# Performance work log

Measured on AMD Instinct MI355X. Metric: run time of the kernel, lower is better.

The kernel has to match this reference:

```python
import jax, jax.numpy as jnp
import numpy as np

INPUT_SIZE = 512
HIDDEN_SIZE = 1024
BATCH = 64
SEQ = 512


def _xavier(key, shape):
    fan_in, fan_out = shape
    limit = float(np.sqrt(6.0 / (fan_in + fan_out)))
    return jax.random.uniform(key, shape, jnp.float32, -limit, limit)


def setup_inputs() -> dict:
    key = jax.random.key(0)
    ks = jax.random.split(key, 9)
    x = jax.random.normal(ks[0], (BATCH, SEQ, INPUT_SIZE), jnp.float32)
    # gate order: i, f, g, o
    W_x = jnp.stack([_xavier(ks[1 + j], (INPUT_SIZE, HIDDEN_SIZE)) for j in range(4)])   # [4, I, H]
    W_h = jnp.stack([_xavier(ks[5 + j], (HIDDEN_SIZE, HIDDEN_SIZE)) for j in range(4)])  # [4, H, H]
    b = jnp.zeros((4, HIDDEN_SIZE), jnp.float32)  # init_weights zeros all biases
    return {"x": x, "W_x": W_x, "W_h": W_h, "b": b}


def reference(x, W_x, W_h, b):
    """x: [B,S,I]; W_x: [4,I,H]; W_h: [4,H,H]; b: [4,H]. Returns final (h, c)."""
    B = x.shape[0]
    H = W_h.shape[-1]
    # Fuse the 4 input-side GEMMs across all timesteps into one big GEMM.
    # xg[t] : [B, 4, H]
    xg = jnp.einsum('bsi,gih->sbgh', x, W_x) + b  # [S, B, 4, H]

    W_h_cat = jnp.transpose(W_h, (1, 0, 2)).reshape(H, 4 * H)  # [H, 4H], gate-major blocks

    def step(carry, xg_t):
        h_prev, c_prev = carry
        gates = xg_t + (h_prev @ W_h_cat).reshape(B, 4, H)  # [B,4,H]
        i_t = jax.nn.sigmoid(gates[:, 0])
        f_t = jax.nn.sigmoid(gates[:, 1])
        g_t = jnp.tanh(gates[:, 2])
        o_t = jax.nn.sigmoid(gates[:, 3])
        c_t = f_t * c_prev + i_t * g_t
        h_t = o_t * jnp.tanh(c_t)
        return (h_t, c_t), None

    h0 = jnp.zeros((B, H), x.dtype)
    c0 = jnp.zeros((B, H), x.dtype)
    (h_T, c_T), _ = jax.lax.scan(step, (h0, c0), xg)
    return h_T, c_T
```

## Files before the change

kernel.cpp:

```cpp
#include <hip/hip_runtime.h>
#include <hip/hip_bf16.h>
#include <stdint.h>
#include <stddef.h>

#define ISZ   512
#define HSZ   1024
#define NBAT  64
#define SEQL  512

typedef __attribute__((ext_vector_type(8))) short  short8;
typedef __attribute__((ext_vector_type(4))) float  floatx4;

__device__ __forceinline__ unsigned short f2bf(float f){
  unsigned int u = __float_as_uint(f);
  u += 0x7FFFu + ((u >> 16) & 1u);
  return (unsigned short)(u >> 16);
}
__device__ __forceinline__ float sigf(float x){ return 1.0f / (1.0f + __expf(-x)); }
__device__ __forceinline__ float tanh_(float x){ return 2.0f / (1.0f + __expf(-2.0f * x)) - 1.0f; }
__device__ __forceinline__ float sel4(int idx, float a0, float a1, float a2, float a3){
  float r01 = (idx & 1) ? a1 : a0;
  float r23 = (idx & 1) ? a3 : a2;
  return (idx & 2) ? r23 : r01;
}

__global__ __launch_bounds__(256) void k_convert_x(const float* __restrict__ x,
                                                   unsigned short* __restrict__ xb,
                                                   int* __restrict__ flags){
  if (blockIdx.x == 0 && threadIdx.x < 256) flags[threadIdx.x] = 0;
  int i = (blockIdx.x * 256 + threadIdx.x) * 8;
  const float4* p = (const float4*)(x + i);
  float4 a = p[0], b = p[1];
  unsigned int w0 = (unsigned int)f2bf(a.x) | ((unsigned int)f2bf(a.y) << 16);
  unsigned int w1 = (unsigned int)f2bf(a.z) | ((unsigned int)f2bf(a.w) << 16);
  unsigned int w2 = (unsigned int)f2bf(b.x) | ((unsigned int)f2bf(b.y) << 16);
  unsigned int w3 = (unsigned int)f2bf(b.z) | ((unsigned int)f2bf(b.w) << 16);
  *(uint4*)(xb + i) = make_uint4(w0, w1, w2, w3);
}

__global__ __launch_bounds__(256) void k_pack_w(const float* __restrict__ Wx,
                                                const float* __restrict__ Wh,
                                                unsigned short* __restrict__ pw){
  int id = blockIdx.x * 256 + threadIdx.x;
  int lane = id & 63;
  int ch   = (id >> 6) % 48;
  int t2   = (id >> 6) / 48;
  int wv = t2 & 3, cg = t2 >> 2;
  int nn = lane & 15, kgrp = lane >> 4;
  int g = nn >> 2, hcl = nn & 3;
  int colh = cg * 16 + wv * 4 + hcl;
  unsigned short o[8];
  if (ch < 32){
    int k0 = ch * 32 + kgrp * 8;
#pragma unroll
    for (int j = 0; j < 8; ++j) o[j] = f2bf(Wh[(g * 1024 + k0 + j) * 1024 + colh]);
  } else {
    int k0 = (ch - 32) * 32 + kgrp * 8;
#pragma unroll
    for (int j = 0; j < 8; ++j) o[j] = f2bf(Wx[(g * 512 + k0 + j) * 1024 + colh]);
  }
  unsigned int w0 = (unsigned int)o[0] | ((unsigned int)o[1] << 16);
  unsigned int w1 = (unsigned int)o[2] | ((unsigned int)o[3] << 16);
  unsigned int w2 = (unsigned int)o[4] | ((unsigned int)o[5] << 16);
  unsigned int w3 = (unsigned int)o[6] | ((unsigned int)o[7] << 16);
  ((uint4*)pw)[id] = make_uint4(w0, w1, w2, w3);
}

__global__ __launch_bounds__(256, 1) void k_scan(const unsigned short* __restrict__ pw,
                                                 const unsigned short* __restrict__ xb,
                                                 const float* __restrict__ bias,
                                                 unsigned long long* __restrict__ hgq,
                                                 int* __restrict__ flags,
                                                 float* __restrict__ out){
  __shared__ __align__(16) char lds_h[16 * 2048];
  __shared__ __align__(16) char lds_x[16 * 1024];

  const int wg = blockIdx.x;
  const int bg = wg >> 6;
  const int cg = wg & 63;
  const int tid = threadIdx.x;
  const int wv = tid >> 6;
  const int lane = tid & 63;
  const int b0 = bg * 16;

  short8 bh[32], bx[16];
  {
    const uint4* base = (const uint4*)pw + (cg * 4 + wv) * 48 * 64 + lane;
#pragma unroll
    for (int c = 0; c < 32; ++c) bh[c] = *(const short8*)(base + c * 64);
#pragma unroll
    for (int c = 0; c < 16; ++c) bx[c] = *(const short8*)(base + (32 + c) * 64);
  }
#pragma unroll
  for (int c = 0; c < 32; ++c) asm volatile("" : "+v"(bh[c]));
#pragma unroll
  for (int c = 0; c < 16; ++c) asm volatile("" : "+v"(bx[c]));

  const int nn = lane & 15;
  const int G  = nn >> 2;
  const int hc = nn & 3;
  const int kgrp = lane >> 4;
  const int colh = cg * 16 + wv * 4 + hc;
  const float b_i = bias[0 * HSZ + colh];
  const float b_f = bias[1 * HSZ + colh];
  const float b_g = bias[2 * HSZ + colh];
  const float b_o = bias[3 * HSZ + colh];

  const int arow = nn;
  const int swz  = (arow & 7) << 4;
  const int hb0  = arow * 2048 + ((kgrp * 16 +  0) ^ swz);
  const int hb1  = arow * 2048 + ((kgrp * 16 + 64) ^ swz);
  const int xq0  = arow * 1024 + ((kgrp * 16 +  0) ^ swz);
  const int xq1  = arow * 1024 + ((kgrp * 16 + 64) ^ swz);

  float cst[4] = {0.f, 0.f, 0.f, 0.f};

#pragma unroll 1
  for (int t = 0; t < SEQL; ++t){
    uint4 xr[4]; int xdst[4];
#pragma unroll
    for (int i = 0; i < 4; ++i){
      int ch = i * 256 + tid;
      int row = ch >> 6, o16 = ch & 63;
      xr[i] = *(const uint4*)((const char*)xb + (((size_t)(b0 + row) * SEQL + t) * ISZ) * 2 + o16 * 16);
      xdst[i] = row * 1024 + ((o16 * 16) ^ ((row & 7) << 4));
    }

    if (t > 0){
      if (wv == 0){
        const int need = 4 * t;
        const int fidx = bg * 64 + lane;
        for (;;){
          int f = __hip_atomic_load(&flags[fidx], __ATOMIC_RELAXED, __HIP_MEMORY_SCOPE_AGENT);
          if (__all(f >= need)) break;
          __builtin_amdgcn_s_sleep(1);
        }
      }
      __syncthreads();
    }

    if (t > 0){
      unsigned long long hr[16]; int hdst[16];
      const int par_r = (t - 1) & 1;
#pragma unroll
      for (int i = 0; i < 16; ++i){
        int ch = i * 256 + tid;
        int row = ch >> 8, o8 = ch & 255;
        hr[i] = __hip_atomic_load(hgq + ((size_t)(par_r * 64 + b0 + row)) * 256 + o8,
                                  __ATOMIC_RELAXED, __HIP_MEMORY_SCOPE_AGENT);
        hdst[i] = row * 2048 + ((o8 * 8) ^ ((row & 7) << 4));
      }
#pragma unroll
      for (int i = 0; i < 16; ++i) *(unsigned long long*)(lds_h + hdst[i]) = hr[i];
    }
#pragma unroll
    for (int i = 0; i < 4; ++i) *(uint4*)(lds_x + xdst[i]) = xr[i];
    __syncthreads();

    floatx4 acc0 = {0.f, 0.f, 0.f, 0.f};
    floatx4 acc1 = {0.f, 0.f, 0.f, 0.f};
    if (t > 0){
#pragma unroll
      for (int q = 0; q < 16; ++q){
        short8 a0 = *(const short8*)(lds_h + hb0 + q * 128);
        acc0 = __builtin_amdgcn_mfma_f32_16x16x32_bf16(a0, bh[2 * q], acc0, 0, 0, 0);
        short8 a1 = *(const short8*)(lds_h + hb1 + q * 128);
        acc1 = __builtin_amdgcn_mfma_f32_16x16x32_bf16(a1, bh[2 * q + 1], acc1, 0, 0, 0);
      }
    }
#pragma unroll
    for (int q = 0; q < 8; ++q){
      short8 a0 = *(const short8*)(lds_x + xq0 + q * 128);
      acc0 = __builtin_amdgcn_mfma_f32_16x16x32_bf16(a0, bx[2 * q], acc0, 0, 0, 0);
      short8 a1 = *(const short8*)(lds_x + xq1 + q * 128);
      acc1 = __builtin_amdgcn_mfma_f32_16x16x32_bf16(a1, bx[2 * q + 1], acc1, 0, 0, 0);
    }

    float hvv[4];
#pragma unroll
    for (int r = 0; r < 4; ++r){
      float own = acc0[r] + acc1[r];
      float s4  = __shfl_xor(own, 4);
      float s8  = __shfl_xor(own, 8);
      float s12 = __shfl_xor(own, 12);
      float pi = sel4(G,     own, s4, s8, s12) + b_i;
      float pf = sel4(G ^ 1, own, s4, s8, s12) + b_f;
      float pg = sel4(G ^ 2, own, s4, s8, s12) + b_g;
      float po = sel4(G ^ 3, own, s4, s8, s12) + b_o;
      float iv = sigf(pi), fv = sigf(pf), gv = tanh_(pg), ov = sigf(po);
      float cn = fv * cst[r] + iv * gv;
      cst[r] = cn;
      hvv[r] = ov * tanh_(cn);
      if (G == 0 && t == SEQL - 1){
        int gb = b0 + kgrp * 4 + r;
        out[gb * HSZ + colh] = hvv[r];
        out[NBAT * HSZ + gb * HSZ + colh] = cn;
      }
    }

    if (G == 0){
      float a0 = hvv[0], a1 = hvv[1], a2 = hvv[2], a3 = hvv[3];
      float s0 = __shfl_xor(a1, 1), s1 = __shfl_xor(a0, 1);
      float s2 = __shfl_xor(a3, 1), s3 = __shfl_xor(a2, 1);
      bool o1 = (nn & 1);
      float t0 = o1 ? s0 : a0,  t1 = o1 ? a1 : s1;
      float t2 = o1 ? s2 : a2,  t3 = o1 ? a3 : s3;
      float u0 = __shfl_xor(t2, 2), u1 = __shfl_xor(t3, 2);
      float u2 = __shfl_xor(t0, 2), u3 = __shfl_xor(t1, 2);
      bool o2 = (nn & 2);
      float w0 = o2 ? u0 : t0,  w1 = o2 ? u1 : t1;
      float w2 = o2 ? t2 : u2,  w3 = o2 ? t3 : u3;
      unsigned int lo = (unsigned int)f2bf(w0) | ((unsigned int)f2bf(w1) << 16);
      unsigned int hi = (unsigned int)f2bf(w2) | ((unsigned int)f2bf(w3) << 16);
      unsigned long long v = ((unsigned long long)hi << 32) | lo;
      int row = kgrp * 4 + nn;
      __hip_atomic_store(hgq + ((size_t)((t & 1) * 64 + b0 + row)) * 256 + (cg * 4 + wv), v,
                         __ATOMIC_RELAXED, __HIP_MEMORY_SCOPE_AGENT);
    }
    asm volatile("s_waitcnt vmcnt(0)" ::: "memory");
    if (lane == 0)
      __hip_atomic_fetch_add(&flags[wg], 1, __ATOMIC_RELAXED, __HIP_MEMORY_SCOPE_AGENT);
  }
}

extern "C" void kernel_launch(void* const* d_in, const int* in_sizes, int n_in,
                              void* d_out, int out_size, void* d_ws, size_t ws_size,
                              hipStream_t stream){
  (void)in_sizes; (void)n_in; (void)out_size; (void)ws_size;
  const float* x  = (const float*)d_in[0];
  const float* Wx = (const float*)d_in[1];
  const float* Wh = (const float*)d_in[2];
  const float* b  = (const float*)d_in[3];
  char* ws = (char*)d_ws;
  unsigned short* pw    = (unsigned short*)ws;
  unsigned short* xbf   = (unsigned short*)(ws + 12582912);
  unsigned long long* hg= (unsigned long long*)(ws + 46137344);
  int*            flags = (int*)(ws + 46399488);
  float* out = (float*)d_out;

  k_convert_x<<<dim3(8192), dim3(256), 0, stream>>>(x, xbf, flags);
  k_pack_w  <<<dim3(3072), dim3(256), 0, stream>>>(Wx, Wh, pw);
  k_scan    <<<dim3(256),  dim3(256), 0, stream>>>(pw, xbf, b, (unsigned long long*)hg, flags, out);
}
```

Measured before the change: 3.157 ms.

## Replace flag-counter barrier with timestep-tagged h exchange and prefetch x projection

The per-step synchronisation changes. Each block no longer bumps a flag counter that consumers poll before loading h. Each bf16 h value is now stored with a 16-bit timestep tag, and consumers spin on the data words until the tags match. The input-projection MFMAs for the next timestep are computed at the end of the current step, which takes them off the h-dependent critical path. The cost is a doubled h exchange footprint. The flag reset also goes away, so stale tags left in the workspace from a previous launch could match early and be read as valid.

After: 7.005 ms. +121.9%, slower.

```diff
diff --git a/kernel.cpp b/kernel.cpp
--- a/kernel.cpp
+++ b/kernel.cpp
@@ -25,9 +25,7 @@
 }
 
 __global__ __launch_bounds__(256) void k_convert_x(const float* __restrict__ x,
-                                                   unsigned short* __restrict__ xb,
-                                                   int* __restrict__ flags){
-  if (blockIdx.x == 0 && threadIdx.x < 256) flags[threadIdx.x] = 0;
+                                                   unsigned short* __restrict__ xb){
   int i = (blockIdx.x * 256 + threadIdx.x) * 8;
   const float4* p = (const float4*)(x + i);
   float4 a = p[0], b = p[1];
@@ -69,8 +67,7 @@
 __global__ __launch_bounds__(256, 1) void k_scan(const unsigned short* __restrict__ pw,
                                                  const unsigned short* __restrict__ xb,
                                                  const float* __restrict__ bias,
-                                                 unsigned long long* __restrict__ hgq,
-                                                 int* __restrict__ flags,
+                                                 unsigned long long* __restrict__ hq,
                                                  float* __restrict__ out){
   __shared__ __align__(16) char lds_h[16 * 2048];
   __shared__ __align__(16) char lds_x[16 * 1024];
@@ -113,52 +110,74 @@
   const int xq0  = arow * 1024 + ((kgrp * 16 +  0) ^ swz);
   const int xq1  = arow * 1024 + ((kgrp * 16 + 64) ^ swz);
 
+  const int prow = tid >> 4;
+  const int pcb  = (tid & 15) * 64;
+  const int pswz = (prow & 7) << 4;
+
   float cst[4] = {0.f, 0.f, 0.f, 0.f};
-
-#pragma unroll 1
-  for (int t = 0; t < SEQL; ++t){
-    uint4 xr[4]; int xdst[4];
+  floatx4 xp0, xp1;
+
+  {
 #pragma unroll
     for (int i = 0; i < 4; ++i){
       int ch = i * 256 + tid;
       int row = ch >> 6, o16 = ch & 63;
-      xr[i] = *(const uint4*)((const char*)xb + (((size_t)(b0 + row) * SEQL + t) * ISZ) * 2 + o16 * 16);
+      uint4 v = *(const uint4*)((const char*)xb + (((size_t)(b0 + row) * SEQL + 0) * ISZ) * 2 + o16 * 16);
+      *(uint4*)(lds_x + row * 1024 + ((o16 * 16) ^ ((row & 7) << 4))) = v;
+    }
+    __syncthreads();
+    floatx4 a0v = {0.f,0.f,0.f,0.f}, a1v = {0.f,0.f,0.f,0.f};
+#pragma unroll
+    for (int q = 0; q < 8; ++q){
+      short8 a0 = *(const short8*)(lds_x + xq0 + q * 128);
+      a0v = __builtin_amdgcn_mfma_f32_16x16x32_bf16(a0, bx[2 * q], a0v, 0, 0, 0);
+      short8 a1 = *(const short8*)(lds_x + xq1 + q * 128);
+      a1v = __builtin_amdgcn_mfma_f32_16x16x32_bf16(a1, bx[2 * q + 1], a1v, 0, 0, 0);
+    }
+    xp0 = a0v; xp1 = a1v;
+    __syncthreads();
+  }
+
+#pragma unroll 1
+  for (int t = 0; t < SEQL; ++t){
+    const int tn = (t + 1 < SEQL) ? (t + 1) : (SEQL - 1);
+    uint4 xr[4]; int xdst[4];
+#pragma unroll
+    for (int i = 0; i < 4; ++i){
+      int ch = i * 256 + tid;
+      int row = ch >> 6, o16 = ch & 63;
+      xr[i] = *(const uint4*)((const char*)xb + (((size_t)(b0 + row) * SEQL + tn) * ISZ) * 2 + o16 * 16);
       xdst[i] = row * 1024 + ((o16 * 16) ^ ((row & 7) << 4));
     }
 
     if (t > 0){
-      if (wv == 0){
-        const int need = 4 * t;
-        const int fidx = bg * 64 + lane;
-        for (;;){
-          int f = __hip_atomic_load(&flags[fidx], __ATOMIC_RELAXED, __HIP_MEMORY_SCOPE_AGENT);
-          if (__all(f >= need)) break;
-          __builtin_amdgcn_s_sleep(1);
+      const unsigned int tg = (unsigned int)(t - 1);
+      unsigned long long* base = hq + ((size_t)(((t - 1) & 1) * 64 + b0 + prow)) * 512 + (pcb >> 1);
+      unsigned long long vals[32];
+      unsigned int pend = 0xFFFFFFFFu;
+      while (pend){
+#pragma unroll
+        for (int q = 0; q < 32; ++q)
+          if ((pend >> q) & 1u)
+            vals[q] = __hip_atomic_load(base + q, __ATOMIC_RELAXED, __HIP_MEMORY_SCOPE_AGENT);
+        unsigned int np = 0;
+#pragma unroll
+        for (int q = 0; q < 32; ++q){
+          if ((pend >> q) & 1u){
+            unsigned int d0 = (unsigned int)vals[q];
+            unsigned int d1 = (unsigned int)(vals[q] >> 32);
+            if ((((d0 >> 16) ^ tg) | ((d1 >> 16) ^ tg)) == 0u){
+              unsigned int packed = (d0 & 0xFFFFu) | (d1 << 16);
+              *(unsigned int*)(lds_h + prow * 2048 + (((pcb + 2 * q) * 2) ^ pswz)) = packed;
+            } else np |= (1u << q);
+          }
         }
+        pend = np;
       }
       __syncthreads();
     }
 
-    if (t > 0){
-      unsigned long long hr[16]; int hdst[16];
-      const int par_r = (t - 1) & 1;
-#pragma unroll
-      for (int i = 0; i < 16; ++i){
-        int ch = i * 256 + tid;
-        int row = ch >> 8, o8 = ch & 255;
-        hr[i] = __hip_atomic_load(hgq + ((size_t)(par_r * 64 + b0 + row)) * 256 + o8,
-                                  __ATOMIC_RELAXED, __HIP_MEMORY_SCOPE_AGENT);
-        hdst[i] = row * 2048 + ((o8 * 8) ^ ((row & 7) << 4));
-      }
-#pragma unroll
-      for (int i = 0; i < 16; ++i) *(unsigned long long*)(lds_h + hdst[i]) = hr[i];
-    }
-#pragma unroll
-    for (int i = 0; i < 4; ++i) *(uint4*)(lds_x + xdst[i]) = xr[i];
-    __syncthreads();
-
-    floatx4 acc0 = {0.f, 0.f, 0.f, 0.f};
-    floatx4 acc1 = {0.f, 0.f, 0.f, 0.f};
+    floatx4 acc0 = xp0, acc1 = xp1;
     if (t > 0){
 #pragma unroll
       for (int q = 0; q < 16; ++q){
@@ -167,13 +186,6 @@
         short8 a1 = *(const short8*)(lds_h + hb1 + q * 128);
         acc1 = __builtin_amdgcn_mfma_f32_16x16x32_bf16(a1, bh[2 * q + 1], acc1, 0, 0, 0);
       }
-    }
-#pragma unroll
-    for (int q = 0; q < 8; ++q){
-      short8 a0 = *(const short8*)(lds_x + xq0 + q * 128);
-      acc0 = __builtin_amdgcn_mfma_f32_16x16x32_bf16(a0, bx[2 * q], acc0, 0, 0, 0);
-      short8 a1 = *(const short8*)(lds_x + xq1 + q * 128);
-      acc1 = __builtin_amdgcn_mfma_f32_16x16x32_bf16(a1, bx[2 * q + 1], acc1, 0, 0, 0);
     }
 
     float hvv[4];
@@ -210,16 +222,34 @@
       bool o2 = (nn & 2);
       float w0 = o2 ? u0 : t0,  w1 = o2 ? u1 : t1;
       float w2 = o2 ? t2 : u2,  w3 = o2 ? t3 : u3;
-      unsigned int lo = (unsigned int)f2bf(w0) | ((unsigned int)f2bf(w1) << 16);
-      unsigned int hi = (unsigned int)f2bf(w2) | ((unsigned int)f2bf(w3) << 16);
-      unsigned long long v = ((unsigned long long)hi << 32) | lo;
+      unsigned int tagw = ((unsigned int)t) << 16;
+      unsigned int p0 = (unsigned int)f2bf(w0) | tagw;
+      unsigned int p1 = (unsigned int)f2bf(w1) | tagw;
+      unsigned int p2 = (unsigned int)f2bf(w2) | tagw;
+      unsigned int p3 = (unsigned int)f2bf(w3) | tagw;
+      unsigned long long v0 = (unsigned long long)p0 | ((unsigned long long)p1 << 32);
+      unsigned long long v1 = (unsigned long long)p2 | ((unsigned long long)p3 << 32);
       int row = kgrp * 4 + nn;
-      __hip_atomic_store(hgq + ((size_t)((t & 1) * 64 + b0 + row)) * 256 + (cg * 4 + wv), v,
-                         __ATOMIC_RELAXED, __HIP_MEMORY_SCOPE_AGENT);
-    }
-    asm volatile("s_waitcnt vmcnt(0)" ::: "memory");
-    if (lane == 0)
-      __hip_atomic_fetch_add(&flags[wg], 1, __ATOMIC_RELAXED, __HIP_MEMORY_SCOPE_AGENT);
+      size_t off = ((size_t)((t & 1) * 64 + b0 + row)) * 512 + cg * 8 + wv * 2;
+      __hip_atomic_store(hq + off,     v0, __ATOMIC_RELAXED, __HIP_MEMORY_SCOPE_AGENT);
+      __hip_atomic_store(hq + off + 1, v1, __ATOMIC_RELAXED, __HIP_MEMORY_SCOPE_AGENT);
+    }
+
+#pragma unroll
+    for (int i = 0; i < 4; ++i) *(uint4*)(lds_x + xdst[i]) = xr[i];
+    __syncthreads();
+    {
+      floatx4 a0v = {0.f,0.f,0.f,0.f}, a1v = {0.f,0.f,0.f,0.f};
+#pragma unroll
+      for (int q = 0; q < 8; ++q){
+        short8 a0 = *(const short8*)(lds_x + xq0 + q * 128);
+        a0v = __builtin_amdgcn_mfma_f32_16x16x32_bf16(a0, bx[2 * q], a0v, 0, 0, 0);
+        short8 a1 = *(const short8*)(lds_x + xq1 + q * 128);
+        a1v = __builtin_amdgcn_mfma_f32_16x16x32_bf16(a1, bx[2 * q + 1], a1v, 0, 0, 0);
+      }
+      xp0 = a0v; xp1 = a1v;
+    }
+    __syncthreads();
   }
 }
 
@@ -232,13 +262,12 @@
   const float* Wh = (const float*)d_in[2];
   const float* b  = (const float*)d_in[3];
   char* ws = (char*)d_ws;
-  unsigned short* pw    = (unsigned short*)ws;
-  unsigned short* xbf   = (unsigned short*)(ws + 12582912);
-  unsigned long long* hg= (unsigned long long*)(ws + 46137344);
-  int*            flags = (int*)(ws + 46399488);
+  unsigned short* pw      = (unsigned short*)ws;
+  unsigned short* xbf     = (unsigned short*)(ws + 12582912);
+  unsigned long long* hq  = (unsigned long long*)(ws + 46137344);
   float* out = (float*)d_out;
 
-  k_convert_x<<<dim3(8192), dim3(256), 0, stream>>>(x, xbf, flags);
+  k_convert_x<<<dim3(8192), dim3(256), 0, stream>>>(x, xbf);
   k_pack_w  <<<dim3(3072), dim3(256), 0, stream>>>(Wx, Wh, pw);
-  k_scan    <<<dim3(256),  dim3(256), 0, stream>>>(pw, xbf, b, (unsigned long long*)hg, flags, out);
-}
+  k_scan    <<<dim3(256),  dim3(256), 0, stream>>>(pw, xbf, b, hq, out);
+}
```
